# Kernel tuning notes

Hardware: AMD Instinct MI355X
Metric: run time of the kernel (lower is better)

The kernel has to match this reference:

```python
import jax, jax.numpy as jnp
import numpy as np

B, N_AA, N_FILT = 2, 20, 12
D, S, C = 64, 512, 1024  # domains, residues per domain, contacts per domain
R = 2 * C                # adjacency rows per domain (contacts * 2)


def setup_inputs() -> dict:
    key = jax.random.key(0)
    k1, k2, k3, k4 = jax.random.split(key, 4)
    aa = jax.random.normal(k1, (B, N_AA, D * S), dtype=jnp.float32)
    adjs = jax.random.uniform(k2, (D, R, S), dtype=jnp.float32)
    w_conv = jax.random.normal(k3, (N_FILT, N_AA, 2), dtype=jnp.float32) * (1.0 / np.sqrt(N_AA * 2))
    w_combine = jax.random.normal(k4, (N_FILT,), dtype=jnp.float32) * (1.0 / np.sqrt(N_FILT))
    return {"aa": aa, "adjs": adjs, "w_conv": w_conv, "w_combine": w_combine}


def reference(aa, adjs, w_conv, w_combine):
    # aa: [B, 20, D*S]; adjs: [D, R, S] with R = 2*C (GAP_LENGTH = 0)
    d, r, s = adjs.shape
    c = r // 2
    aa_d = aa.reshape(aa.shape[0], aa.shape[1], d, s)          # split into domains
    # _expand: per-domain aa_chunk @ adj.T -> [D, B, 20, R]
    x = jnp.einsum('bcds,drs->dbcr', aa_d, adjs)
    # spatial_conv: Conv1d(20->12, k=2, stride=2, no bias); even chunk lengths
    # mean windows never cross domain boundaries -> pair-reshape + contract
    xp = x.reshape(d, aa.shape[0], aa.shape[1], c, 2)           # [D,B,20,C,2]
    h = jnp.einsum('dbcpk,fck->dbfp', xp, w_conv)               # [D,B,12,C]
    # _contract: h @ adj[::2, :] -> [D, B, 12, S]
    y = jnp.einsum('dbfp,dps->dbfs', h, adjs[:, ::2, :])
    # _agg_by_domain: degree-normalized max-pool over residues, then linear
    deg = adjs.sum(axis=1)                                      # [D, S]
    pooled = (y / deg[:, None, None, :]).max(axis=3)            # [D, B, 12]
    scores = jnp.einsum('dbf,f->db', pooled, w_combine)         # [D, B]
    return jax.nn.sigmoid(scores.reshape(-1))                   # cat over domains -> [D*B]
```

## Files before the change

### kernel.cpp

```cpp
#include <hip/hip_runtime.h>
#include <math.h>

#define D_DOM 64
#define S_RES 512
#define R_ROWS 2048
#define NAA 20
#define NF 12
#define NB 2
#define NJ 24
#define NPC 8
#define BROWS 8
#define NBATCH 32
#define BSTR 520

typedef unsigned short ushort_t;
typedef unsigned int uint_t;
typedef short bf16x8 __attribute__((ext_vector_type(8)));
typedef float f32x4 __attribute__((ext_vector_type(4)));

__device__ __forceinline__ ushort_t f2bf(float x) {
  uint_t u = __float_as_uint(x);
  uint_t r = u + 0x7FFFu + ((u >> 16) & 1u);
  return (ushort_t)(r >> 16);
}
__device__ __forceinline__ float bflo(uint_t u) { return __uint_as_float(u << 16); }
__device__ __forceinline__ float bfhi(uint_t u) { return __uint_as_float(u & 0xFFFF0000u); }
__device__ __forceinline__ uint_t pk2(float a, float b) {
  return (uint_t)f2bf(a) | ((uint_t)f2bf(b) << 16);
}

__device__ __forceinline__ void gload_lds16(const float* g, float* l) {
  __builtin_amdgcn_global_load_lds((const __attribute__((address_space(1))) void*)g,
                                   (__attribute__((address_space(3))) void*)l,
                                   16, 0, 0);
}

__global__ __launch_bounds__(256) void kA_g(const float* __restrict__ aa,
                                            const float* __restrict__ wconv,
                                            ushort_t* __restrict__ g) {
  __shared__ float ws[NF * NAA * 2];
  const int tid = threadIdx.x;
  for (int i = tid; i < NF * NAA * 2; i += 256) ws[i] = wconv[i];
  __syncthreads();
  const int pos = blockIdx.x * 256 + tid;
  const int b = blockIdx.y;
  float av[NAA];
#pragma unroll
  for (int c = 0; c < NAA; ++c)
    av[c] = aa[(size_t)(b * NAA + c) * (D_DOM * S_RES) + pos];
  const int d = pos >> 9;
  const int s = pos & 511;
#pragma unroll
  for (int f = 0; f < NF; ++f) {
    float s0 = 0.f, s1 = 0.f;
#pragma unroll
    for (int c = 0; c < NAA; ++c) {
      const float a = av[c];
      s0 = fmaf(a, ws[(f * NAA + c) * 2 + 0], s0);
      s1 = fmaf(a, ws[(f * NAA + c) * 2 + 1], s1);
    }
    const int j = b * NF + f;
    g[((size_t)(d * NJ + j)) * 1024 + s] = f2bf(s0);
    g[((size_t)(d * NJ + j)) * 1024 + 512 + s] = f2bf(s1);
  }
}

__global__ __launch_bounds__(256) void kB_main(const float* __restrict__ adjs,
                                               const ushort_t* __restrict__ g,
                                               ushort_t* __restrict__ yp,
                                               float* __restrict__ degp) {
  const int tid = threadIdx.x;
  const int w = tid >> 6;
  const int l = tid & 63;
  const int d = blockIdx.x >> 3;
  const int pc = blockIdx.x & 7;

  const int mt = w & 1, kh = w >> 1;
  const int jl = l & 15, kg = l >> 4;
  const int pl = jl & 3;

  __shared__ float rows[2][BROWS][S_RES];
  __shared__ __align__(16) ushort_t Bs16[2][BROWS][BSTR];
  __shared__ __align__(16) float hs[2][2][2][16][4];

  const float* ablk = adjs + ((size_t)d * R_ROWS + (size_t)pc * 256) * S_RES;

  bf16x8 gf[16];
  {
    const int j_a = mt * 16 + jl;
    const bool valid = (j_a < NJ);
    const ushort_t* gr =
        g + ((size_t)(d * NJ + (valid ? j_a : 0))) * 1024 + kh * 512 + kg * 8;
    const bf16x8 z = {};
#pragma unroll
    for (int ks = 0; ks < 16; ++ks) {
      bf16x8 v = *(const bf16x8*)(gr + ks * 32);
      gf[ks] = valid ? v : z;
    }
  }

  float yv[6][8];
#pragma unroll
  for (int jj = 0; jj < 6; ++jj)
#pragma unroll
    for (int e = 0; e < 8; ++e) yv[jj][e] = 0.f;
  float dgv[8];
#pragma unroll
  for (int e = 0; e < 8; ++e) dgv[e] = 0.f;

#define STAGE(T)                                                               \
  {                                                                            \
    _Pragma("unroll")                                                          \
    for (int q = 0; q < 4; ++q) {                                              \
      const int u_ = w * 4 + q;                                                \
      const int row_ = u_ >> 1;                                                \
      const int half_ = u_ & 1;                                                \
      gload_lds16(ablk + ((size_t)((T)*BROWS + row_)) * S_RES + half_ * 256 +  \
                      l * 4,                                                   \
                  &rows[(T) & 1][row_][half_ * 256]);                          \
    }                                                                          \
  }

#define Y_PHASE(TT)                                                            \
  {                                                                            \
    const int buf_ = (TT) & 1;                                                 \
    float ae[4][8];                                                            \
    _Pragma("unroll") for (int p = 0; p < 4; ++p) {                            \
      const uint4 v = *(const uint4*)&Bs16[buf_][p * 2][l * 8];                \
      ae[p][0] = bflo(v.x); ae[p][1] = bfhi(v.x);                              \
      ae[p][2] = bflo(v.y); ae[p][3] = bfhi(v.y);                              \
      ae[p][4] = bflo(v.z); ae[p][5] = bfhi(v.z);                              \
      ae[p][6] = bflo(v.w); ae[p][7] = bfhi(v.w);                              \
    }                                                                          \
    _Pragma("unroll") for (int jj = 0; jj < 6; ++jj) {                         \
      const int j_ = w * 6 + jj;                                               \
      const int jt_ = j_ >> 4, jlo_ = j_ & 15;                                 \
      const f32x4 ha = *(const f32x4*)&hs[buf_][0][jt_][jlo_][0];              \
      const f32x4 hb = *(const f32x4*)&hs[buf_][1][jt_][jlo_][0];              \
      const f32x4 h4 = ha + hb;                                                \
      _Pragma("unroll") for (int p = 0; p < 4; ++p) {                          \
        const float hv = h4[p];                                                \
        _Pragma("unroll") for (int e = 0; e < 8; ++e)                          \
            yv[jj][e] = fmaf(hv, ae[p][e], yv[jj][e]);                         \
      }                                                                        \
    }                                                                          \
  }

  STAGE(0);

  for (int t = 0; t < NBATCH; ++t) {
    asm volatile("s_waitcnt vmcnt(0)" ::: "memory");
    asm volatile("s_waitcnt lgkmcnt(0)\n\ts_barrier" ::: "memory");
    if (t + 1 < NBATCH) STAGE(t + 1);

    {
      const int r_ = tid >> 5;
      const int c0 = (tid & 31) * 16;
      const float4 a = *(const float4*)&rows[t & 1][r_][c0];
      const float4 b = *(const float4*)&rows[t & 1][r_][c0 + 4];
      const float4 c = *(const float4*)&rows[t & 1][r_][c0 + 8];
      const float4 e = *(const float4*)&rows[t & 1][r_][c0 + 12];
      uint4 o0, o1;
      o0.x = pk2(a.x, a.y); o0.y = pk2(a.z, a.w);
      o0.z = pk2(b.x, b.y); o0.w = pk2(b.z, b.w);
      o1.x = pk2(c.x, c.y); o1.y = pk2(c.z, c.w);
      o1.z = pk2(e.x, e.y); o1.w = pk2(e.z, e.w);
      *(uint4*)&Bs16[t & 1][r_][c0] = o0;
      *(uint4*)&Bs16[t & 1][r_][c0 + 8] = o1;
    }

    if (t) Y_PHASE(t - 1);

    asm volatile("s_waitcnt lgkmcnt(0)\n\ts_barrier" ::: "memory");

#pragma unroll
    for (int rr = 0; rr < 2; ++rr) {
      const uint4 v = *(const uint4*)&Bs16[t & 1][2 * w + rr][l * 8];
      dgv[0] += bflo(v.x); dgv[1] += bfhi(v.x);
      dgv[2] += bflo(v.y); dgv[3] += bfhi(v.y);
      dgv[4] += bflo(v.z); dgv[5] += bfhi(v.z);
      dgv[6] += bflo(v.w); dgv[7] += bfhi(v.w);
    }

    {
      f32x4 acc = {0.f, 0.f, 0.f, 0.f};
#pragma unroll
      for (int ks = 0; ks < 16; ++ks) {
        const bf16x8 bfr =
            *(const bf16x8*)&Bs16[t & 1][pl * 2 + kh][ks * 32 + kg * 8];
        acc = __builtin_amdgcn_mfma_f32_16x16x32_bf16(gf[ks], bfr, acc, 0, 0, 0);
      }
      if (jl < 4) {
#pragma unroll
        for (int i = 0; i < 4; ++i) hs[t & 1][kh][mt][kg * 4 + i][jl] = acc[i];
      }
    }
  }

  asm volatile("s_waitcnt lgkmcnt(0)\n\ts_barrier" ::: "memory");
  Y_PHASE(NBATCH - 1);

  ushort_t* ypb = yp + (size_t)(pc * D_DOM + d) * NJ * S_RES;
#pragma unroll
  for (int jj = 0; jj < 6; ++jj) {
    const int j = w * 6 + jj;
    uint4 o;
    o.x = pk2(yv[jj][0], yv[jj][1]);
    o.y = pk2(yv[jj][2], yv[jj][3]);
    o.z = pk2(yv[jj][4], yv[jj][5]);
    o.w = pk2(yv[jj][6], yv[jj][7]);
    *(uint4*)(ypb + (size_t)j * S_RES + l * 8) = o;
  }
  {
    float* dp = degp + (((size_t)(d * NPC + pc)) * 4 + w) * S_RES + l * 8;
    *(float4*)dp = make_float4(dgv[0], dgv[1], dgv[2], dgv[3]);
    *(float4*)(dp + 4) = make_float4(dgv[4], dgv[5], dgv[6], dgv[7]);
  }
}

__global__ __launch_bounds__(256) void kD0_rdeg(const float* __restrict__ degp,
                                                float* __restrict__ rdeg) {
  const int d = blockIdx.x;
  const int tid = threadIdx.x;
  float dg0 = 0.f, dg1 = 0.f;
  const float* base = degp + (size_t)d * NPC * 4 * S_RES;
#pragma unroll 8
  for (int k = 0; k < NPC * 4; ++k) {
    const float2 dv = *(const float2*)(base + (size_t)k * S_RES + 2 * tid);
    dg0 += dv.x;
    dg1 += dv.y;
  }
  *(float2*)(rdeg + (size_t)d * S_RES + 2 * tid) = make_float2(1.f / dg0, 1.f / dg1);
}

__global__ __launch_bounds__(256) void kD1_pool(const ushort_t* __restrict__ yp,
                                                const float* __restrict__ rdeg,
                                                float* __restrict__ pool) {
  const int j = blockIdx.x;
  const int d = blockIdx.y;
  const int tid = threadIdx.x;
  __shared__ float wmax[4];

  float v0 = 0.f, v1 = 0.f;
#pragma unroll
  for (int pc = 0; pc < NPC; ++pc) {
    const ushort2 yv =
        *(const ushort2*)(yp + ((size_t)(pc * D_DOM + d) * NJ + j) * S_RES + 2 * tid);
    v0 += __uint_as_float((uint_t)yv.x << 16);
    v1 += __uint_as_float((uint_t)yv.y << 16);
  }
  const float2 rv = *(const float2*)(rdeg + (size_t)d * S_RES + 2 * tid);
  float m = fmaxf(v0 * rv.x, v1 * rv.y);
#pragma unroll
  for (int mask = 32; mask; mask >>= 1) m = fmaxf(m, __shfl_xor(m, mask));
  if ((tid & 63) == 0) wmax[tid >> 6] = m;
  __syncthreads();
  if (tid == 0)
    pool[d * NJ + j] = fmaxf(fmaxf(wmax[0], wmax[1]), fmaxf(wmax[2], wmax[3]));
}

__global__ __launch_bounds__(128) void kD2_out(const float* __restrict__ pool,
                                               const float* __restrict__ wcomb,
                                               float* __restrict__ out) {
  const int t = threadIdx.x;
  if (t < D_DOM * NB) {
    const int d = t >> 1, b = t & 1;
    float sc = 0.f;
#pragma unroll
    for (int f = 0; f < NF; ++f) sc = fmaf(pool[d * NJ + b * NF + f], wcomb[f], sc);
    out[t] = 1.0f / (1.0f + expf(-sc));
  }
}

extern "C" void kernel_launch(void* const* d_in, const int* in_sizes, int n_in,
                              void* d_out, int out_size, void* d_ws, size_t ws_size,
                              hipStream_t stream) {
  const float* aa = (const float*)d_in[0];
  const float* adjs = (const float*)d_in[1];
  const float* wconv = (const float*)d_in[2];
  const float* wcomb = (const float*)d_in[3];
  float* out = (float*)d_out;
  char* wsb = (char*)d_ws;

  ushort_t* g = (ushort_t*)wsb;
  ushort_t* yp = (ushort_t*)(wsb + 3145728);
  float* degp = (float*)(wsb + 15728640);
  float* rdeg = (float*)(wsb + 19922944);
  float* pool = (float*)(wsb + 20054016);

  kA_g<<<dim3(128, 2), dim3(256), 0, stream>>>(aa, wconv, g);
  kB_main<<<dim3(512), dim3(256), 0, stream>>>(adjs, g, yp, degp);
  kD0_rdeg<<<dim3(64), dim3(256), 0, stream>>>(degp, rdeg);
  kD1_pool<<<dim3(24, 64), dim3(256), 0, stream>>>(yp, rdeg, pool);
  kD2_out<<<dim3(1), dim3(128), 0, stream>>>(pool, wcomb, out);
}
```

Before: 94.70 us.

## Batch 32 adjacency rows per MFMA step and fuse tail kernels

The main kernel now converts four 8-row sub-batches into a 32-row bf16 LDS buffer before each MFMA pass. That makes all 16 MFMA output columns useful and cuts barriers per row. Global-to-LDS loads are kept two sub-batches ahead using partial vmcnt waits. Degree sums are now taken from the fp32 rows instead of the bf16 copies. The three reduction/output kernels are merged into one per-domain kernel that does pooling and the sigmoid, which removes launches but gives less parallelism in that stage (64 blocks).

```diff
diff --git a/kernel.cpp b/kernel.cpp
--- a/kernel.cpp
+++ b/kernel.cpp
@@ -9,8 +9,9 @@
 #define NB 2
 #define NJ 24
 #define NPC 8
-#define BROWS 8
-#define NBATCH 32
+#define SUB 8
+#define NSUB 32
+#define NSB 8
 #define BSTR 520
 
 typedef unsigned short ushort_t;
@@ -25,6 +26,9 @@
 }
 __device__ __forceinline__ float bflo(uint_t u) { return __uint_as_float(u << 16); }
 __device__ __forceinline__ float bfhi(uint_t u) { return __uint_as_float(u & 0xFFFF0000u); }
+__device__ __forceinline__ float bf2f(ushort_t h) {
+  return __uint_as_float(((uint_t)h) << 16);
+}
 __device__ __forceinline__ uint_t pk2(float a, float b) {
   return (uint_t)f2bf(a) | ((uint_t)f2bf(b) << 16);
 }
@@ -77,11 +81,10 @@
 
   const int mt = w & 1, kh = w >> 1;
   const int jl = l & 15, kg = l >> 4;
-  const int pl = jl & 3;
-
-  __shared__ float rows[2][BROWS][S_RES];
-  __shared__ __align__(16) ushort_t Bs16[2][BROWS][BSTR];
-  __shared__ __align__(16) float hs[2][2][2][16][4];
+
+  __shared__ float rows[2][SUB][S_RES];
+  __shared__ __align__(16) ushort_t Bs16[4 * SUB][BSTR];
+  __shared__ __align__(16) float hs[2][32][16];
 
   const float* ablk = adjs + ((size_t)d * R_ROWS + (size_t)pc * 256) * S_RES;
 
@@ -99,106 +102,109 @@
     }
   }
 
-  float yv[6][8];
-#pragma unroll
-  for (int jj = 0; jj < 6; ++jj)
-#pragma unroll
-    for (int e = 0; e < 8; ++e) yv[jj][e] = 0.f;
-  float dgv[8];
-#pragma unroll
-  for (int e = 0; e < 8; ++e) dgv[e] = 0.f;
-
-#define STAGE(T)                                                               \
+#define STAGE(SB)                                                              \
   {                                                                            \
     _Pragma("unroll")                                                          \
     for (int q = 0; q < 4; ++q) {                                              \
       const int u_ = w * 4 + q;                                                \
       const int row_ = u_ >> 1;                                                \
       const int half_ = u_ & 1;                                                \
-      gload_lds16(ablk + ((size_t)((T)*BROWS + row_)) * S_RES + half_ * 256 +  \
+      gload_lds16(ablk + ((size_t)((SB)*SUB + row_)) * S_RES + half_ * 256 +   \
                       l * 4,                                                   \
-                  &rows[(T) & 1][row_][half_ * 256]);                          \
+                  &rows[(SB) & 1][row_][half_ * 256]);                         \
     }                                                                          \
   }
 
-#define Y_PHASE(TT)                                                            \
-  {                                                                            \
-    const int buf_ = (TT) & 1;                                                 \
-    float ae[4][8];                                                            \
-    _Pragma("unroll") for (int p = 0; p < 4; ++p) {                            \
-      const uint4 v = *(const uint4*)&Bs16[buf_][p * 2][l * 8];                \
-      ae[p][0] = bflo(v.x); ae[p][1] = bfhi(v.x);                              \
-      ae[p][2] = bflo(v.y); ae[p][3] = bfhi(v.y);                              \
-      ae[p][4] = bflo(v.z); ae[p][5] = bfhi(v.z);                              \
-      ae[p][6] = bflo(v.w); ae[p][7] = bfhi(v.w);                              \
-    }                                                                          \
-    _Pragma("unroll") for (int jj = 0; jj < 6; ++jj) {                         \
-      const int j_ = w * 6 + jj;                                               \
-      const int jt_ = j_ >> 4, jlo_ = j_ & 15;                                 \
-      const f32x4 ha = *(const f32x4*)&hs[buf_][0][jt_][jlo_][0];              \
-      const f32x4 hb = *(const f32x4*)&hs[buf_][1][jt_][jlo_][0];              \
-      const f32x4 h4 = ha + hb;                                                \
-      _Pragma("unroll") for (int p = 0; p < 4; ++p) {                          \
-        const float hv = h4[p];                                                \
-        _Pragma("unroll") for (int e = 0; e < 8; ++e)                          \
-            yv[jj][e] = fmaf(hv, ae[p][e], yv[jj][e]);                         \
-      }                                                                        \
-    }                                                                          \
-  }
-
   STAGE(0);
-
-  for (int t = 0; t < NBATCH; ++t) {
-    asm volatile("s_waitcnt vmcnt(0)" ::: "memory");
+  STAGE(1);
+  asm volatile("s_waitcnt vmcnt(0)" ::: "memory");
+
+  float yv[6][8];
+#pragma unroll
+  for (int jj = 0; jj < 6; ++jj)
+#pragma unroll
+    for (int e = 0; e < 8; ++e) yv[jj][e] = 0.f;
+  float dg[16];
+#pragma unroll
+  for (int e = 0; e < 16; ++e) dg[e] = 0.f;
+
+  const int r_ = tid >> 5;
+  const int c0 = (tid & 31) * 16;
+
+  for (int T = 0; T < NSB; ++T) {
+#pragma unroll
+    for (int u = 0; u < 4; ++u) {
+      const int sb = T * 4 + u;
+      if (sb >= 2) {
+        if (sb < NSUB - 1) {
+          asm volatile("s_waitcnt vmcnt(4)" ::: "memory");
+        } else {
+          asm volatile("s_waitcnt vmcnt(0)" ::: "memory");
+        }
+      }
+      {
+        const float4 a = *(const float4*)&rows[sb & 1][r_][c0];
+        const float4 b = *(const float4*)&rows[sb & 1][r_][c0 + 4];
+        const float4 c = *(const float4*)&rows[sb & 1][r_][c0 + 8];
+        const float4 e = *(const float4*)&rows[sb & 1][r_][c0 + 12];
+        dg[0] += a.x;  dg[1] += a.y;  dg[2] += a.z;  dg[3] += a.w;
+        dg[4] += b.x;  dg[5] += b.y;  dg[6] += b.z;  dg[7] += b.w;
+        dg[8] += c.x;  dg[9] += c.y;  dg[10] += c.z; dg[11] += c.w;
+        dg[12] += e.x; dg[13] += e.y; dg[14] += e.z; dg[15] += e.w;
+        uint4 o0, o1;
+        o0.x = pk2(a.x, a.y); o0.y = pk2(a.z, a.w);
+        o0.z = pk2(b.x, b.y); o0.w = pk2(b.z, b.w);
+        o1.x = pk2(c.x, c.y); o1.y = pk2(c.z, c.w);
+        o1.z = pk2(e.x, e.y); o1.w = pk2(e.z, e.w);
+        *(uint4*)&Bs16[u * SUB + r_][c0] = o0;
+        *(uint4*)&Bs16[u * SUB + r_][c0 + 8] = o1;
+      }
+      if (sb + 2 < NSUB) STAGE(sb + 2);
+    }
+
     asm volatile("s_waitcnt lgkmcnt(0)\n\ts_barrier" ::: "memory");
-    if (t + 1 < NBATCH) STAGE(t + 1);
-
-    {
-      const int r_ = tid >> 5;
-      const int c0 = (tid & 31) * 16;
-      const float4 a = *(const float4*)&rows[t & 1][r_][c0];
-      const float4 b = *(const float4*)&rows[t & 1][r_][c0 + 4];
-      const float4 c = *(const float4*)&rows[t & 1][r_][c0 + 8];
-      const float4 e = *(const float4*)&rows[t & 1][r_][c0 + 12];
-      uint4 o0, o1;
-      o0.x = pk2(a.x, a.y); o0.y = pk2(a.z, a.w);
-      o0.z = pk2(b.x, b.y); o0.w = pk2(b.z, b.w);
-      o1.x = pk2(c.x, c.y); o1.y = pk2(c.z, c.w);
-      o1.z = pk2(e.x, e.y); o1.w = pk2(e.z, e.w);
-      *(uint4*)&Bs16[t & 1][r_][c0] = o0;
-      *(uint4*)&Bs16[t & 1][r_][c0 + 8] = o1;
-    }
-
-    if (t) Y_PHASE(t - 1);
-
-    asm volatile("s_waitcnt lgkmcnt(0)\n\ts_barrier" ::: "memory");
-
-#pragma unroll
-    for (int rr = 0; rr < 2; ++rr) {
-      const uint4 v = *(const uint4*)&Bs16[t & 1][2 * w + rr][l * 8];
-      dgv[0] += bflo(v.x); dgv[1] += bfhi(v.x);
-      dgv[2] += bflo(v.y); dgv[3] += bfhi(v.y);
-      dgv[4] += bflo(v.z); dgv[5] += bfhi(v.z);
-      dgv[6] += bflo(v.w); dgv[7] += bfhi(v.w);
-    }
 
     {
       f32x4 acc = {0.f, 0.f, 0.f, 0.f};
 #pragma unroll
       for (int ks = 0; ks < 16; ++ks) {
-        const bf16x8 bfr =
-            *(const bf16x8*)&Bs16[t & 1][pl * 2 + kh][ks * 32 + kg * 8];
+        const bf16x8 bfr = *(const bf16x8*)&Bs16[2 * jl + kh][ks * 32 + kg * 8];
         acc = __builtin_amdgcn_mfma_f32_16x16x32_bf16(gf[ks], bfr, acc, 0, 0, 0);
       }
-      if (jl < 4) {
-#pragma unroll
-        for (int i = 0; i < 4; ++i) hs[t & 1][kh][mt][kg * 4 + i][jl] = acc[i];
-      }
-    }
-  }
-
-  asm volatile("s_waitcnt lgkmcnt(0)\n\ts_barrier" ::: "memory");
-  Y_PHASE(NBATCH - 1);
+#pragma unroll
+      for (int i = 0; i < 4; ++i) hs[kh][mt * 16 + kg * 4 + i][jl] = acc[i];
+    }
+
+    asm volatile("s_waitcnt lgkmcnt(0)\n\ts_barrier" ::: "memory");
+
+#pragma unroll
+    for (int pg = 0; pg < 4; ++pg) {
+      float ae[4][8];
+#pragma unroll
+      for (int q = 0; q < 4; ++q) {
+        const uint4 v = *(const uint4*)&Bs16[2 * (pg * 4 + q)][l * 8];
+        ae[q][0] = bflo(v.x); ae[q][1] = bfhi(v.x);
+        ae[q][2] = bflo(v.y); ae[q][3] = bfhi(v.y);
+        ae[q][4] = bflo(v.z); ae[q][5] = bfhi(v.z);
+        ae[q][6] = bflo(v.w); ae[q][7] = bfhi(v.w);
+      }
+#pragma unroll
+      for (int jj = 0; jj < 6; ++jj) {
+        const int j_ = w * 6 + jj;
+        const f32x4 ha = *(const f32x4*)&hs[0][j_][pg * 4];
+        const f32x4 hb = *(const f32x4*)&hs[1][j_][pg * 4];
+        const f32x4 h4 = ha + hb;
+#pragma unroll
+        for (int q = 0; q < 4; ++q) {
+          const float hv = h4[q];
+#pragma unroll
+          for (int e = 0; e < 8; ++e) yv[jj][e] = fmaf(hv, ae[q][e], yv[jj][e]);
+        }
+      }
+    }
+
+    asm volatile("s_waitcnt lgkmcnt(0)\n\ts_barrier" ::: "memory");
+  }
 
   ushort_t* ypb = yp + (size_t)(pc * D_DOM + d) * NJ * S_RES;
 #pragma unroll
@@ -212,63 +218,58 @@
     *(uint4*)(ypb + (size_t)j * S_RES + l * 8) = o;
   }
   {
-    float* dp = degp + (((size_t)(d * NPC + pc)) * 4 + w) * S_RES + l * 8;
-    *(float4*)dp = make_float4(dgv[0], dgv[1], dgv[2], dgv[3]);
-    *(float4*)(dp + 4) = make_float4(dgv[4], dgv[5], dgv[6], dgv[7]);
-  }
-}
-
-__global__ __launch_bounds__(256) void kD0_rdeg(const float* __restrict__ degp,
-                                                float* __restrict__ rdeg) {
+    float* dp = degp + (((size_t)(d * NPC + pc)) * 8 + r_) * S_RES + c0;
+    *(float4*)dp = make_float4(dg[0], dg[1], dg[2], dg[3]);
+    *(float4*)(dp + 4) = make_float4(dg[4], dg[5], dg[6], dg[7]);
+    *(float4*)(dp + 8) = make_float4(dg[8], dg[9], dg[10], dg[11]);
+    *(float4*)(dp + 12) = make_float4(dg[12], dg[13], dg[14], dg[15]);
+  }
+}
+
+__global__ __launch_bounds__(256) void kDf(const ushort_t* __restrict__ yp,
+                                           const float* __restrict__ degp,
+                                           const float* __restrict__ wcomb,
+                                           float* __restrict__ out) {
   const int d = blockIdx.x;
   const int tid = threadIdx.x;
+  const int tj = tid >> 6;
+  __shared__ float wm[NJ][4];
+  __shared__ float pool[NJ];
+
   float dg0 = 0.f, dg1 = 0.f;
-  const float* base = degp + (size_t)d * NPC * 4 * S_RES;
+  const float* base = degp + (size_t)d * NPC * 8 * S_RES;
 #pragma unroll 8
-  for (int k = 0; k < NPC * 4; ++k) {
+  for (int k = 0; k < NPC * 8; ++k) {
     const float2 dv = *(const float2*)(base + (size_t)k * S_RES + 2 * tid);
     dg0 += dv.x;
     dg1 += dv.y;
   }
-  *(float2*)(rdeg + (size_t)d * S_RES + 2 * tid) = make_float2(1.f / dg0, 1.f / dg1);
-}
-
-__global__ __launch_bounds__(256) void kD1_pool(const ushort_t* __restrict__ yp,
-                                                const float* __restrict__ rdeg,
-                                                float* __restrict__ pool) {
-  const int j = blockIdx.x;
-  const int d = blockIdx.y;
-  const int tid = threadIdx.x;
-  __shared__ float wmax[4];
-
-  float v0 = 0.f, v1 = 0.f;
-#pragma unroll
-  for (int pc = 0; pc < NPC; ++pc) {
-    const ushort2 yv =
-        *(const ushort2*)(yp + ((size_t)(pc * D_DOM + d) * NJ + j) * S_RES + 2 * tid);
-    v0 += __uint_as_float((uint_t)yv.x << 16);
-    v1 += __uint_as_float((uint_t)yv.y << 16);
-  }
-  const float2 rv = *(const float2*)(rdeg + (size_t)d * S_RES + 2 * tid);
-  float m = fmaxf(v0 * rv.x, v1 * rv.y);
-#pragma unroll
-  for (int mask = 32; mask; mask >>= 1) m = fmaxf(m, __shfl_xor(m, mask));
-  if ((tid & 63) == 0) wmax[tid >> 6] = m;
+  const float q0 = 1.0f / dg0;
+  const float q1 = 1.0f / dg1;
+
+  for (int j = 0; j < NJ; ++j) {
+    float v0 = 0.f, v1 = 0.f;
+#pragma unroll
+    for (int pc = 0; pc < NPC; ++pc) {
+      const ushort2 yv =
+          *(const ushort2*)(yp + ((size_t)(pc * D_DOM + d) * NJ + j) * S_RES + 2 * tid);
+      v0 += bf2f(yv.x);
+      v1 += bf2f(yv.y);
+    }
+    float m = fmaxf(v0 * q0, v1 * q1);
+#pragma unroll
+    for (int mask = 32; mask; mask >>= 1) m = fmaxf(m, __shfl_xor(m, mask));
+    if ((tid & 63) == 0) wm[j][tj] = m;
+  }
   __syncthreads();
-  if (tid == 0)
-    pool[d * NJ + j] = fmaxf(fmaxf(wmax[0], wmax[1]), fmaxf(wmax[2], wmax[3]));
-}
-
-__global__ __launch_bounds__(128) void kD2_out(const float* __restrict__ pool,
-                                               const float* __restrict__ wcomb,
-                                               float* __restrict__ out) {
-  const int t = threadIdx.x;
-  if (t < D_DOM * NB) {
-    const int d = t >> 1, b = t & 1;
+  if (tid < NJ)
+    pool[tid] = fmaxf(fmaxf(wm[tid][0], wm[tid][1]), fmaxf(wm[tid][2], wm[tid][3]));
+  __syncthreads();
+  if (tid < NB) {
     float sc = 0.f;
 #pragma unroll
-    for (int f = 0; f < NF; ++f) sc = fmaf(pool[d * NJ + b * NF + f], wcomb[f], sc);
-    out[t] = 1.0f / (1.0f + expf(-sc));
+    for (int f = 0; f < NF; ++f) sc = fmaf(pool[tid * NF + f], wcomb[f], sc);
+    out[d * NB + tid] = 1.0f / (1.0f + expf(-sc));
   }
 }
 
@@ -285,12 +286,8 @@
   ushort_t* g = (ushort_t*)wsb;
   ushort_t* yp = (ushort_t*)(wsb + 3145728);
   float* degp = (float*)(wsb + 15728640);
-  float* rdeg = (float*)(wsb + 19922944);
-  float* pool = (float*)(wsb + 20054016);
 
   kA_g<<<dim3(128, 2), dim3(256), 0, stream>>>(aa, wconv, g);
   kB_main<<<dim3(512), dim3(256), 0, stream>>>(adjs, g, yp, degp);
-  kD0_rdeg<<<dim3(64), dim3(256), 0, stream>>>(degp, rdeg);
-  kD1_pool<<<dim3(24, 64), dim3(256), 0, stream>>>(yp, rdeg, pool);
-  kD2_out<<<dim3(1), dim3(128), 0, stream>>>(pool, wcomb, out);
-}
+  kDf<<<dim3(64), dim3(256), 0, stream>>>(yp, degp, wcomb, out);
+}
```

Result: slower. 125.1 us (+32.1%).
